# Kernel optimization log

Hardware: AMD Instinct MI355X
Metric: run time of the kernel (lower is better)

The kernel has to match this reference:

```python
import jax, jax.numpy as jnp
import numpy as np

K = 3          # kernel_size
DIL = 2        # dilation
PAD = 2        # padding = dilation*(K-1)/2 so output spatial == input spatial
RANKS = 3
EPS = 1e-6


def _unfold(h):
    """Replicate-pad then extract KxK dilated patches -> (b, c, K*K, H, W).
    Kernel-position ordering matches torch.nn.Unfold (row-major kh*K+kw)."""
    b, c, H, W = h.shape
    p = jnp.pad(h, ((0, 0), (0, 0), (PAD, PAD), (PAD, PAD)), mode='edge')
    patches = [p[:, :, i * DIL:i * DIL + H, j * DIL:j * DIL + W]
               for i in range(K) for j in range(K)]
    return jnp.stack(patches, axis=2)  # (b, c, K*K, H, W)


def setup_inputs() -> dict:
    key = jax.random.key(0)
    k1, k2, k3 = jax.random.split(key, 3)
    B, C, H, W = 4, 64, 128, 128
    x = jax.random.normal(k1, (B, C, H, W), dtype=jnp.float32)
    W_head = jax.random.normal(k2, (64, 64), dtype=jnp.float32) * 0.05  # (out_c, in_c)
    W_tail = jax.random.normal(k3, (64, 64), dtype=jnp.float32) * 0.05  # (in_c, out_c)
    return {"x": x, "W_head": W_head, "W_tail": W_tail}


def reference(x, W_head, W_tail):
    res = x
    # 1x1 head conv (no bias) + ReLU
    h = jax.nn.relu(jnp.einsum('oc,bchw->bohw', W_head, x))
    # im2col: (b, C, K*K, H, W)
    X = _unfold(h)
    # NMF-style init: broadcast means over kernel / channel dims to rank r
    U = jnp.repeat(X.mean(axis=2, keepdims=True), RANKS, axis=2)  # (b,c,r,h,w)
    V = jnp.repeat(X.mean(axis=1, keepdims=True), RANKS, axis=1)  # (b,r,k,h,w)
    # one Lee-Seung multiplicative update (stage_num=1)
    num = jnp.einsum('bcrhw,bckhw->brkhw', U, X)
    den = jnp.einsum('bcrhw,bckhw->brkhw', U,
                     jnp.einsum('bcrhw,brkhw->bckhw', U, V))
    V = V * (num / (den + EPS))
    num = jnp.einsum('bckhw,brkhw->bcrhw', X, V)
    den = jnp.einsum('bckhw,brkhw->bcrhw',
                     jnp.einsum('bcrhw,brkhw->bckhw', U, V), V)
    U = U * (num / (den + EPS))
    center = (K // 2) * K + K // 2  # = 4
    UV = jnp.einsum('bcrhw,brkhw->bckhw', U, V[:, :, center:center + 1])[:, :, 0]
    out = jnp.einsum('co,bohw->bchw', W_tail, UV) + res
    return out
```

## Files before the change

kernel.cpp:

```cpp
#include <hip/hip_runtime.h>

#define HWC 16384
#define WD  128
#define NC  64
#define EPSV 1e-6f

typedef __attribute__((ext_vector_type(8))) short bf16x8;
typedef __attribute__((ext_vector_type(4))) float f32x4;

__device__ __forceinline__ unsigned short f2bf(float f) {
  unsigned u = __builtin_bit_cast(unsigned, f);
  u = (u + 0x7FFFu + ((u >> 16) & 1u)) >> 16;
  return (unsigned short)u;
}
__device__ __forceinline__ float bf2f(unsigned short h) {
  return __builtin_bit_cast(float, ((unsigned)h) << 16);
}
__device__ __forceinline__ float bfLo(unsigned pk) { return __builtin_bit_cast(float, pk << 16); }
__device__ __forceinline__ float bfHi(unsigned pk) { return __builtin_bit_cast(float, pk & 0xFFFF0000u); }
__device__ __forceinline__ int swz(int row, int colbytes) {
  return ((row << 7) + colbytes) ^ ((row & 7) << 4);
}
__device__ __forceinline__ bf16x8 pack8(float4 a, float4 b) {
  bf16x8 r;
  r[0] = (short)f2bf(a.x); r[1] = (short)f2bf(a.y);
  r[2] = (short)f2bf(a.z); r[3] = (short)f2bf(a.w);
  r[4] = (short)f2bf(b.x); r[5] = (short)f2bf(b.y);
  r[6] = (short)f2bf(b.z); r[7] = (short)f2bf(b.w);
  return r;
}

__global__ __launch_bounds__(512, 4) void k_fused(const float* __restrict__ x,
                                                  const float* __restrict__ Wh,
                                                  const float* __restrict__ Wt,
                                                  float* __restrict__ out) {
  __shared__ __align__(16) char smem[53760];
  unsigned short* xt = (unsigned short*)smem;
  unsigned short* hl = (unsigned short*)(smem + 26624);
  float* red = (float*)smem;
  unsigned short* uvb = (unsigned short*)smem;

  const int t = threadIdx.x, lane = t & 63, wv = t >> 6;
  const int bid0 = blockIdx.x;
  const int bid = ((bid0 & 7) << 7) | (bid0 >> 3);
  const int seg = bid & 1, y = (bid >> 1) & 127, b = bid >> 8;
  const int w0 = seg << 6;
  const int c0 = wv << 3;
  const int l15 = lane & 15, kg = lane >> 4;
  const int mt = wv & 3;
  const int mrow = (mt << 4) + l15;

  int gy[3];
  gy[0] = y >= 2 ? y - 2 : 0;
  gy[1] = y;
  gy[2] = y <= 125 ? y + 2 : 127;

  const float* xb = x + (size_t)b * (NC * HWC);

  bf16x8 ha0, ha1;
  {
    const float* wr = Wh + mrow * 64 + kg * 8;
    ha0 = pack8(*(const float4*)wr, *(const float4*)(wr + 4));
    ha1 = pack8(*(const float4*)(wr + 32), *(const float4*)(wr + 36));
  }

  {
    int colm = w0 - 2 + lane; if (colm < 0) colm = 0;
#pragma unroll
    for (int r = 0; r < 3; ++r) {
      const float* xr = xb + gy[r] * WD;
      const int srow = r * 68 + lane;
#pragma unroll
      for (int q = 0; q < 2; ++q) {
        unsigned long long pk = 0;
#pragma unroll
        for (int u = 0; u < 4; ++u)
          pk |= (unsigned long long)f2bf(xr[(size_t)(c0 + q * 4 + u) * HWC + colm]) << (16 * u);
        *(unsigned long long*)((char*)xt + swz(srow, (c0 + q * 4) * 2)) = pk;
      }
    }
    if (lane < 12) {
      const int re = lane >> 2, e = lane & 3;
      int cole = w0 + 62 + e; if (cole > 127) cole = 127;
      const float* xr = xb + gy[re] * WD;
      const int srow = re * 68 + 64 + e;
#pragma unroll
      for (int q = 0; q < 2; ++q) {
        unsigned long long pk = 0;
#pragma unroll
        for (int u = 0; u < 4; ++u)
          pk |= (unsigned long long)f2bf(xr[(size_t)(c0 + q * 4 + u) * HWC + cole]) << (16 * u);
        *(unsigned long long*)((char*)xt + swz(srow, (c0 + q * 4) * 2)) = pk;
      }
    }
  }
  __syncthreads();

  {
    const int ntBeg = (wv >> 2) ? 7 : 0;
    const int ntEnd = (wv >> 2) ? 13 : 7;
    const f32x4 z = {0.f, 0.f, 0.f, 0.f};
    for (int nt = ntBeg; nt < ntEnd; ++nt) {
      const int s = (nt << 4) + l15;
      const bf16x8 b0 = *(const bf16x8*)((char*)xt + swz(s, kg * 16));
      const bf16x8 b1 = *(const bf16x8*)((char*)xt + swz(s, 64 + kg * 16));
      f32x4 acc = __builtin_amdgcn_mfma_f32_16x16x32_bf16(ha0, b0, z, 0, 0, 0);
      acc = __builtin_amdgcn_mfma_f32_16x16x32_bf16(ha1, b1, acc, 0, 0, 0);
#pragma unroll
      for (int j = 0; j < 4; ++j) {
        const int c2 = (mt << 4) + kg * 4 + j;
        float v = acc[j];
        v = v > 0.f ? v : 0.f;
        hl[c2 * 212 + s] = f2bf(v);
      }
    }
  }
  __syncthreads();

  float S = 0.f, sumk[9], A[9], mreg[8];
  unsigned tp[8][5];
#pragma unroll
  for (int k = 0; k < 9; ++k) { sumk[k] = 0.f; A[k] = 0.f; }
#pragma unroll
  for (int i = 0; i < 8; ++i) {
    const int hb2 = (c0 + i) * 212 + lane;
    unsigned short t9[9];
#pragma unroll
    for (int r = 0; r < 3; ++r) {
#pragma unroll
      for (int k = 0; k < 3; ++k) t9[3 * r + k] = hl[hb2 + r * 68 + 2 * k];
    }
    tp[i][0] = (unsigned)t9[0] | ((unsigned)t9[1] << 16);
    tp[i][1] = (unsigned)t9[2] | ((unsigned)t9[3] << 16);
    tp[i][2] = (unsigned)t9[4] | ((unsigned)t9[5] << 16);
    tp[i][3] = (unsigned)t9[6] | ((unsigned)t9[7] << 16);
    tp[i][4] = (unsigned)t9[8];
    float tap[9];
#pragma unroll
    for (int k = 0; k < 9; ++k) tap[k] = bf2f(t9[k]);
    float m = 0.f;
#pragma unroll
    for (int k = 0; k < 9; ++k) m += tap[k];
    m *= (1.f / 9.f);
    mreg[i] = m;
    S += m * m;
#pragma unroll
    for (int k = 0; k < 9; ++k) { sumk[k] += tap[k]; A[k] += m * tap[k]; }
  }
  __syncthreads();

  {
    const int rb = t * 21;
    red[rb + 0] = S;
#pragma unroll
    for (int k = 0; k < 9; ++k) red[rb + 1 + k] = sumk[k];
#pragma unroll
    for (int k = 0; k < 9; ++k) red[rb + 10 + k] = A[k];
  }
  __syncthreads();

  for (int q = wv; q < 19; q += 8) {
    float f = 0.f;
#pragma unroll
    for (int w = 0; w < 8; ++w) f += red[(w * 64 + lane) * 21 + q];
    red[lane * 21 + q] = f;
  }
  __syncthreads();

  float Vk[9], T = 0.f;
  {
    const int rb = lane * 21;
    const float Sf = red[rb + 0];
#pragma unroll
    for (int k = 0; k < 9; ++k) {
      const float sk = red[rb + 1 + k];
      const float Ak = red[rb + 10 + k];
      const float nk = sk * (1.f / 64.f);
      Vk[k] = nk * (Ak / (3.f * nk * Sf + EPSV));
      T += Vk[k] * Vk[k];
    }
  }
  const float V4 = Vk[4];
  __syncthreads();

  bf16x8 ta0, ta1;
  {
    const float* wr = Wt + mrow * 64 + kg * 8;
    ta0 = pack8(*(const float4*)wr, *(const float4*)(wr + 4));
    ta1 = pack8(*(const float4*)(wr + 32), *(const float4*)(wr + 36));
  }

#pragma unroll
  for (int i = 0; i < 8; i += 2) {
    unsigned short pk[2];
#pragma unroll
    for (int u = 0; u < 2; ++u) {
      float Bc = 0.f;
      Bc += bfLo(tp[i + u][0]) * Vk[0];
      Bc += bfHi(tp[i + u][0]) * Vk[1];
      Bc += bfLo(tp[i + u][1]) * Vk[2];
      Bc += bfHi(tp[i + u][1]) * Vk[3];
      Bc += bfLo(tp[i + u][2]) * Vk[4];
      Bc += bfHi(tp[i + u][2]) * Vk[5];
      Bc += bfLo(tp[i + u][3]) * Vk[6];
      Bc += bfHi(tp[i + u][3]) * Vk[7];
      Bc += bfLo(tp[i + u][4]) * Vk[8];
      const float m = mreg[i + u];
      const float Uc = m * (Bc / (3.f * m * T + EPSV));
      pk[u] = f2bf(3.f * Uc * V4);
    }
    const unsigned w32 = (unsigned)pk[0] | ((unsigned)pk[1] << 16);
    *(unsigned*)((char*)uvb + swz(lane, (c0 + i) * 2)) = w32;
  }
  __syncthreads();

  const int n0 = (wv >> 2) << 1;
  const f32x4 z = {0.f, 0.f, 0.f, 0.f};
  const size_t gb = (size_t)b * (NC * HWC) + (size_t)y * WD + w0;
#pragma unroll
  for (int nt = n0; nt < n0 + 2; ++nt) {
    const int px = (nt << 4) + l15;
    const bf16x8 b0 = *(const bf16x8*)((char*)uvb + swz(px, kg * 16));
    const bf16x8 b1 = *(const bf16x8*)((char*)uvb + swz(px, 64 + kg * 16));
    f32x4 acc = __builtin_amdgcn_mfma_f32_16x16x32_bf16(ta0, b0, z, 0, 0, 0);
    acc = __builtin_amdgcn_mfma_f32_16x16x32_bf16(ta1, b1, acc, 0, 0, 0);
#pragma unroll
    for (int j = 0; j < 4; ++j) {
      const int c2 = (mt << 4) + kg * 4 + j;
      const size_t off = gb + (size_t)c2 * HWC + px;
      out[off] = acc[j] + x[off];
    }
  }
}

extern "C" void kernel_launch(void* const* d_in, const int* in_sizes, int n_in,
                              void* d_out, int out_size, void* d_ws, size_t ws_size,
                              hipStream_t stream) {
  const float* x  = (const float*)d_in[0];
  const float* Wh = (const float*)d_in[1];
  const float* Wt = (const float*)d_in[2];
  float* out = (float*)d_out;

  k_fused<<<1024, 512, 0, stream>>>(x, Wh, Wt, out);
}
```

Before: 28.10 us.

## Store head activations pixel-major swizzled and read taps as 128-bit LDS vectors

Changes the LDS layout of the ReLU'd head output from channel-major scalar bf16 entries to a pixel-major swizzled layout. The tap gather then uses nine 16-byte vector loads per thread instead of 72 scalar short loads, and the MFMA epilogue writes packed 8-byte stores. The x staging now writes one 16-byte store per row, and the reduction buffer is padded to 22 floats so float2 accesses can be used. The intent is to cut LDS instruction count and bank conflicts; the cost is keeping more tap registers live, which may raise register pressure.

```diff
diff --git a/kernel.cpp b/kernel.cpp
--- a/kernel.cpp
+++ b/kernel.cpp
@@ -7,14 +7,12 @@
 
 typedef __attribute__((ext_vector_type(8))) short bf16x8;
 typedef __attribute__((ext_vector_type(4))) float f32x4;
+typedef __attribute__((ext_vector_type(4))) unsigned int u32x4;
 
 __device__ __forceinline__ unsigned short f2bf(float f) {
   unsigned u = __builtin_bit_cast(unsigned, f);
   u = (u + 0x7FFFu + ((u >> 16) & 1u)) >> 16;
   return (unsigned short)u;
-}
-__device__ __forceinline__ float bf2f(unsigned short h) {
-  return __builtin_bit_cast(float, ((unsigned)h) << 16);
 }
 __device__ __forceinline__ float bfLo(unsigned pk) { return __builtin_bit_cast(float, pk << 16); }
 __device__ __forceinline__ float bfHi(unsigned pk) { return __builtin_bit_cast(float, pk & 0xFFFF0000u); }
@@ -34,7 +32,7 @@
                                                   const float* __restrict__ Wh,
                                                   const float* __restrict__ Wt,
                                                   float* __restrict__ out) {
-  __shared__ __align__(16) char smem[53760];
+  __shared__ __align__(16) char smem[53248];
   unsigned short* xt = (unsigned short*)smem;
   unsigned short* hl = (unsigned short*)(smem + 26624);
   float* red = (float*)smem;
@@ -68,30 +66,20 @@
     int colm = w0 - 2 + lane; if (colm < 0) colm = 0;
 #pragma unroll
     for (int r = 0; r < 3; ++r) {
-      const float* xr = xb + gy[r] * WD;
-      const int srow = r * 68 + lane;
-#pragma unroll
-      for (int q = 0; q < 2; ++q) {
-        unsigned long long pk = 0;
-#pragma unroll
-        for (int u = 0; u < 4; ++u)
-          pk |= (unsigned long long)f2bf(xr[(size_t)(c0 + q * 4 + u) * HWC + colm]) << (16 * u);
-        *(unsigned long long*)((char*)xt + swz(srow, (c0 + q * 4) * 2)) = pk;
-      }
+      const float* xr = xb + gy[r] * WD + colm;
+      bf16x8 v;
+#pragma unroll
+      for (int u = 0; u < 8; ++u) v[u] = (short)f2bf(xr[(size_t)(c0 + u) * HWC]);
+      *(bf16x8*)((char*)xt + swz(r * 68 + lane, c0 * 2)) = v;
     }
     if (lane < 12) {
       const int re = lane >> 2, e = lane & 3;
       int cole = w0 + 62 + e; if (cole > 127) cole = 127;
-      const float* xr = xb + gy[re] * WD;
-      const int srow = re * 68 + 64 + e;
-#pragma unroll
-      for (int q = 0; q < 2; ++q) {
-        unsigned long long pk = 0;
-#pragma unroll
-        for (int u = 0; u < 4; ++u)
-          pk |= (unsigned long long)f2bf(xr[(size_t)(c0 + q * 4 + u) * HWC + cole]) << (16 * u);
-        *(unsigned long long*)((char*)xt + swz(srow, (c0 + q * 4) * 2)) = pk;
-      }
+      const float* xr = xb + gy[re] * WD + cole;
+      bf16x8 v;
+#pragma unroll
+      for (int u = 0; u < 8; ++u) v[u] = (short)f2bf(xr[(size_t)(c0 + u) * HWC]);
+      *(bf16x8*)((char*)xt + swz(re * 68 + 64 + e, c0 * 2)) = v;
     }
   }
   __syncthreads();
@@ -106,77 +94,87 @@
       const bf16x8 b1 = *(const bf16x8*)((char*)xt + swz(s, 64 + kg * 16));
       f32x4 acc = __builtin_amdgcn_mfma_f32_16x16x32_bf16(ha0, b0, z, 0, 0, 0);
       acc = __builtin_amdgcn_mfma_f32_16x16x32_bf16(ha1, b1, acc, 0, 0, 0);
-#pragma unroll
-      for (int j = 0; j < 4; ++j) {
-        const int c2 = (mt << 4) + kg * 4 + j;
-        float v = acc[j];
-        v = v > 0.f ? v : 0.f;
-        hl[c2 * 212 + s] = f2bf(v);
-      }
-    }
-  }
-  __syncthreads();
+      const float v0 = acc[0] > 0.f ? acc[0] : 0.f;
+      const float v1 = acc[1] > 0.f ? acc[1] : 0.f;
+      const float v2 = acc[2] > 0.f ? acc[2] : 0.f;
+      const float v3 = acc[3] > 0.f ? acc[3] : 0.f;
+      uint2 pk2;
+      pk2.x = (unsigned)f2bf(v0) | ((unsigned)f2bf(v1) << 16);
+      pk2.y = (unsigned)f2bf(v2) | ((unsigned)f2bf(v3) << 16);
+      *(uint2*)((char*)hl + swz(s, (mt * 16 + kg * 4) * 2)) = pk2;
+    }
+  }
+  __syncthreads();
+
+  const int pl = lane;
+  u32x4 tap[9];
+#pragma unroll
+  for (int r = 0; r < 3; ++r)
+#pragma unroll
+    for (int kc = 0; kc < 3; ++kc)
+      tap[r * 3 + kc] = *(const u32x4*)((char*)hl + swz(r * 68 + pl + 2 * kc, c0 * 2));
 
   float S = 0.f, sumk[9], A[9], mreg[8];
-  unsigned tp[8][5];
 #pragma unroll
   for (int k = 0; k < 9; ++k) { sumk[k] = 0.f; A[k] = 0.f; }
 #pragma unroll
-  for (int i = 0; i < 8; ++i) {
-    const int hb2 = (c0 + i) * 212 + lane;
-    unsigned short t9[9];
-#pragma unroll
-    for (int r = 0; r < 3; ++r) {
-#pragma unroll
-      for (int k = 0; k < 3; ++k) t9[3 * r + k] = hl[hb2 + r * 68 + 2 * k];
-    }
-    tp[i][0] = (unsigned)t9[0] | ((unsigned)t9[1] << 16);
-    tp[i][1] = (unsigned)t9[2] | ((unsigned)t9[3] << 16);
-    tp[i][2] = (unsigned)t9[4] | ((unsigned)t9[5] << 16);
-    tp[i][3] = (unsigned)t9[6] | ((unsigned)t9[7] << 16);
-    tp[i][4] = (unsigned)t9[8];
-    float tap[9];
-#pragma unroll
-    for (int k = 0; k < 9; ++k) tap[k] = bf2f(t9[k]);
+  for (int c = 0; c < 8; ++c) {
+    float tc[9];
+#pragma unroll
+    for (int k = 0; k < 9; ++k) {
+      const unsigned w32 = tap[k][c >> 1];
+      tc[k] = (c & 1) ? bfHi(w32) : bfLo(w32);
+    }
     float m = 0.f;
 #pragma unroll
-    for (int k = 0; k < 9; ++k) m += tap[k];
+    for (int k = 0; k < 9; ++k) m += tc[k];
     m *= (1.f / 9.f);
-    mreg[i] = m;
+    mreg[c] = m;
     S += m * m;
 #pragma unroll
-    for (int k = 0; k < 9; ++k) { sumk[k] += tap[k]; A[k] += m * tap[k]; }
-  }
-  __syncthreads();
-
-  {
-    const int rb = t * 21;
-    red[rb + 0] = S;
-#pragma unroll
-    for (int k = 0; k < 9; ++k) red[rb + 1 + k] = sumk[k];
-#pragma unroll
-    for (int k = 0; k < 9; ++k) red[rb + 10 + k] = A[k];
-  }
-  __syncthreads();
-
-  for (int q = wv; q < 19; q += 8) {
-    float f = 0.f;
-#pragma unroll
-    for (int w = 0; w < 8; ++w) f += red[(w * 64 + lane) * 21 + q];
-    red[lane * 21 + q] = f;
+    for (int k = 0; k < 9; ++k) { sumk[k] += tc[k]; A[k] += m * tc[k]; }
+  }
+  __syncthreads();
+
+  {
+    float2* cell = (float2*)&red[t * 22];
+    cell[0] = make_float2(S, sumk[0]);
+    cell[1] = make_float2(sumk[1], sumk[2]);
+    cell[2] = make_float2(sumk[3], sumk[4]);
+    cell[3] = make_float2(sumk[5], sumk[6]);
+    cell[4] = make_float2(sumk[7], sumk[8]);
+    cell[5] = make_float2(A[0], A[1]);
+    cell[6] = make_float2(A[2], A[3]);
+    cell[7] = make_float2(A[4], A[5]);
+    cell[8] = make_float2(A[6], A[7]);
+    red[t * 22 + 18] = A[8];
+  }
+  __syncthreads();
+
+  for (int p = wv; p < 10; p += 8) {
+    float2 f = {0.f, 0.f};
+#pragma unroll
+    for (int w2 = 0; w2 < 8; ++w2) {
+      const float2 g = *(const float2*)&red[(w2 * 64 + lane) * 22 + 2 * p];
+      f.x += g.x; f.y += g.y;
+    }
+    *(float2*)&red[lane * 22 + 2 * p] = f;
   }
   __syncthreads();
 
   float Vk[9], T = 0.f;
   {
-    const int rb = lane * 21;
-    const float Sf = red[rb + 0];
+    const float2* cell = (const float2*)&red[lane * 22];
+    const float2 d0 = cell[0], d1 = cell[1], d2 = cell[2], d3 = cell[3], d4 = cell[4];
+    const float2 d5 = cell[5], d6 = cell[6], d7 = cell[7], d8 = cell[8];
+    const float a8 = red[lane * 22 + 18];
+    const float Sf = d0.x;
+    const float sk[9] = {d0.y, d1.x, d1.y, d2.x, d2.y, d3.x, d3.y, d4.x, d4.y};
+    const float Ak[9] = {d5.x, d5.y, d6.x, d6.y, d7.x, d7.y, d8.x, d8.y, a8};
 #pragma unroll
     for (int k = 0; k < 9; ++k) {
-      const float sk = red[rb + 1 + k];
-      const float Ak = red[rb + 10 + k];
-      const float nk = sk * (1.f / 64.f);
-      Vk[k] = nk * (Ak / (3.f * nk * Sf + EPSV));
+      const float nk = sk[k] * (1.f / 64.f);
+      Vk[k] = nk * (Ak[k] / (3.f * nk * Sf + EPSV));
       T += Vk[k] * Vk[k];
     }
   }
@@ -190,39 +188,34 @@
     ta1 = pack8(*(const float4*)(wr + 32), *(const float4*)(wr + 36));
   }
 
-#pragma unroll
-  for (int i = 0; i < 8; i += 2) {
-    unsigned short pk[2];
-#pragma unroll
-    for (int u = 0; u < 2; ++u) {
+  {
+    bf16x8 vv;
+#pragma unroll
+    for (int c = 0; c < 8; ++c) {
       float Bc = 0.f;
-      Bc += bfLo(tp[i + u][0]) * Vk[0];
-      Bc += bfHi(tp[i + u][0]) * Vk[1];
-      Bc += bfLo(tp[i + u][1]) * Vk[2];
-      Bc += bfHi(tp[i + u][1]) * Vk[3];
-      Bc += bfLo(tp[i + u][2]) * Vk[4];
-      Bc += bfHi(tp[i + u][2]) * Vk[5];
-      Bc += bfLo(tp[i + u][3]) * Vk[6];
-      Bc += bfHi(tp[i + u][3]) * Vk[7];
-      Bc += bfLo(tp[i + u][4]) * Vk[8];
-      const float m = mreg[i + u];
+#pragma unroll
+      for (int k = 0; k < 9; ++k) {
+        const unsigned w32 = tap[k][c >> 1];
+        const float tk = (c & 1) ? bfHi(w32) : bfLo(w32);
+        Bc += tk * Vk[k];
+      }
+      const float m = mreg[c];
       const float Uc = m * (Bc / (3.f * m * T + EPSV));
-      pk[u] = f2bf(3.f * Uc * V4);
-    }
-    const unsigned w32 = (unsigned)pk[0] | ((unsigned)pk[1] << 16);
-    *(unsigned*)((char*)uvb + swz(lane, (c0 + i) * 2)) = w32;
+      vv[c] = (short)f2bf(3.f * Uc * V4);
+    }
+    *(bf16x8*)((char*)uvb + swz(pl, c0 * 2)) = vv;
   }
   __syncthreads();
 
   const int n0 = (wv >> 2) << 1;
-  const f32x4 z = {0.f, 0.f, 0.f, 0.f};
+  const f32x4 z2 = {0.f, 0.f, 0.f, 0.f};
   const size_t gb = (size_t)b * (NC * HWC) + (size_t)y * WD + w0;
 #pragma unroll
   for (int nt = n0; nt < n0 + 2; ++nt) {
     const int px = (nt << 4) + l15;
     const bf16x8 b0 = *(const bf16x8*)((char*)uvb + swz(px, kg * 16));
     const bf16x8 b1 = *(const bf16x8*)((char*)uvb + swz(px, 64 + kg * 16));
-    f32x4 acc = __builtin_amdgcn_mfma_f32_16x16x32_bf16(ta0, b0, z, 0, 0, 0);
+    f32x4 acc = __builtin_amdgcn_mfma_f32_16x16x32_bf16(ta0, b0, z2, 0, 0, 0);
     acc = __builtin_amdgcn_mfma_f32_16x16x32_bf16(ta1, b1, acc, 0, 0, 0);
 #pragma unroll
     for (int j = 0; j < 4; ++j) {
```

After: 27.12 us. 1.04x faster.
